# Optimization experiments

Hardware: AMD Instinct MI355X
Metric: run time of the kernel (lower is better)

Reference implementation:

```python
import jax, jax.numpy as jnp
import numpy as np

B, T, SDIM, NIV = 8192, 128, 6, 6
ENC = 16            # features per microstructure encoder
MDIM = 2 * ENC      # 32
HID = 256
DT = 0.01
IN_DIM = SDIM * 2 + NIV + MDIM  # 50


def _lin_init(key, fan_in, fan_out):
    # torch nn.Linear default: U(-1/sqrt(fan_in), 1/sqrt(fan_in)); stored as [in, out]
    k1, k2 = jax.random.split(key)
    bound = 1.0 / np.sqrt(fan_in)
    W = jax.random.uniform(k1, (fan_in, fan_out), jnp.float32, -bound, bound)
    b = jax.random.uniform(k2, (fan_out,), jnp.float32, -bound, bound)
    return W, b


def setup_inputs() -> dict:
    key = jax.random.key(0)
    ks = jax.random.split(key, 10)
    e = jax.random.normal(ks[0], (B, T, SDIM), jnp.float32)
    e_dot = jax.random.normal(ks[1], (B, T, SDIM), jnp.float32)
    E = jax.random.uniform(ks[2], (B, 1), jnp.float32)
    nu = jax.random.uniform(ks[3], (B, 1), jnp.float32)
    We, be = _lin_init(ks[4], 1, ENC)
    Wn, bn = _lin_init(ks[5], 1, ENC)
    Wen1, ben1 = _lin_init(ks[6], IN_DIM, HID)
    Wen2, ben2 = _lin_init(ks[7], HID, 1)
    Wd1, bd1 = _lin_init(ks[8], IN_DIM, HID)
    Wd2, bd2 = _lin_init(ks[9], HID, NIV)
    return {"e": e, "e_dot": e_dot, "E": E, "nu": nu,
            "We": We, "be": be, "Wn": Wn, "bn": bn,
            "Wen1": Wen1, "ben1": ben1, "Wen2": Wen2, "ben2": ben2,
            "Wd1": Wd1, "bd1": bd1, "Wd2": Wd2, "bd2": bd2}


def _mlp(x, W1, b1, W2, b2):
    return jnp.maximum(x @ W1 + b1, 0.0) @ W2 + b2


def reference(e, e_dot, E, nu, We, be, Wn, bn, Wen1, ben1, Wen2, ben2, Wd1, bd1, Wd2, bd2):
    # microstructure features; original recomputes every step but inputs are constant
    mf = jnp.concatenate([E @ We + be, nu @ Wn + bn], axis=-1)  # [B, MDIM]
    e_t = jnp.moveaxis(e, 1, 0)        # [T, B, SDIM]
    ed_t = jnp.moveaxis(e_dot, 1, 0)   # [T, B, SDIM]
    xi0 = jnp.zeros((e.shape[0], NIV), e.dtype)

    def step(xi, inp):
        et, edt = inp
        x = jnp.concatenate([et, edt, xi, mf], axis=-1)       # [B, IN_DIM]
        s = _mlp(x, Wen1, ben1, Wen2, ben2)[..., 0]           # [B] energy -> stress
        kin = _mlp(x, Wd1, bd1, Wd2, bd2)                     # [B, NIV]
        return xi + DT * kin, (s, xi)  # explicit Euler update; emit xi BEFORE update

    _, (stress, xi_all) = jax.lax.scan(step, xi0, (e_t, ed_t))
    # stress: [T, B] -> [B, T]; xi_all: [T, B, NIV] -> [B, T, NIV] (xi[:,0] == 0)
    return jnp.moveaxis(stress, 0, 1), jnp.moveaxis(xi_all, 0, 1)
```

## Files before the change

kernel.cpp:

```cpp
#include <hip/hip_runtime.h>

#define BN   8192
#define TN   128
#define HIDN 256
#define DTC  0.01f

typedef float v2f __attribute__((ext_vector_type(2)));

#define DPP_ADD(v, ctrl, rmask)                                                 \
    v += __int_as_float(__builtin_amdgcn_update_dpp(                            \
            0, __float_as_int(v), ctrl, rmask, 0xf, true))

#define WAVE_SUM(v) do {                                                        \
    DPP_ADD(v, 0x111, 0xf);                                     \
    DPP_ADD(v, 0x112, 0xf);                                     \
    DPP_ADD(v, 0x114, 0xf);                                     \
    DPP_ADD(v, 0x118, 0xf);            \
    DPP_ADD(v, 0x142, 0xa);   \
    DPP_ADD(v, 0x143, 0xc);              \
} while (0)

#define LANE_SUM(v) __int_as_float(__builtin_amdgcn_readlane(__float_as_int(v), 63))

__global__ __launch_bounds__(256, 2)
void visco_kernel(const float* __restrict__ e,    const float* __restrict__ ed,
                  const float* __restrict__ Earr, const float* __restrict__ nuarr,
                  const float* __restrict__ We,   const float* __restrict__ be,
                  const float* __restrict__ Wn,   const float* __restrict__ bn,
                  const float* __restrict__ Wen1, const float* __restrict__ ben1,
                  const float* __restrict__ Wen2, const float* __restrict__ ben2,
                  const float* __restrict__ Wd1,  const float* __restrict__ bd1,
                  const float* __restrict__ Wd2,  const float* __restrict__ bd2,
                  float* __restrict__ out)
{
    const int lane = threadIdx.x & 63;
    const int wv   = threadIdx.x >> 6;
    const int b    = (blockIdx.x << 2) + wv;

    v2f   wP[2][4][9];
    float cst[2][4];
    float w2s[4];
    float w2k[4][6];

    const float Eb  = Earr[b];
    const float nub = nuarr[b];

    #pragma unroll
    for (int u = 0; u < 4; ++u) {
        const int j = (u << 6) + lane;
        #pragma unroll
        for (int kk = 0; kk < 9; ++kk) {
            wP[0][u][kk] = v2f{Wen1[(2 * kk) * HIDN + j], Wen1[(2 * kk + 1) * HIDN + j]};
            wP[1][u][kk] = v2f{Wd1 [(2 * kk) * HIDN + j], Wd1 [(2 * kk + 1) * HIDN + j]};
        }
        float c0 = ben1[j];
        float c1 = bd1[j];
        #pragma unroll
        for (int k = 0; k < 16; ++k) {
            const float m = fmaf(Eb, We[k], be[k]);
            c0 = fmaf(m, Wen1[(18 + k) * HIDN + j], c0);
            c1 = fmaf(m, Wd1 [(18 + k) * HIDN + j], c1);
        }
        #pragma unroll
        for (int k = 0; k < 16; ++k) {
            const float m = fmaf(nub, Wn[k], bn[k]);
            c0 = fmaf(m, Wen1[(34 + k) * HIDN + j], c0);
            c1 = fmaf(m, Wd1 [(34 + k) * HIDN + j], c1);
        }
        cst[0][u] = c0;
        cst[1][u] = c1;
        w2s[u] = Wen2[j];
        #pragma unroll
        for (int i = 0; i < 6; ++i) w2k[u][i] = Wd2[j * 6 + i];
    }

    const float ben2v = ben2[0];
    float bd2v[6];
    #pragma unroll
    for (int i = 0; i < 6; ++i) bd2v[i] = bd2[i];

    v2f xi01 = v2f{0.f, 0.f}, xi23 = v2f{0.f, 0.f}, xi45 = v2f{0.f, 0.f};

    const v2f* ep = (const v2f*)(e  + (size_t)b * (TN * 6));
    const v2f* dp = (const v2f*)(ed + (size_t)b * (TN * 6));
    float* outS = out + (size_t)b * TN;
    float* outX = out + (size_t)BN * TN + (size_t)b * (TN * 6);

    v2f e0 = ep[0], e1 = ep[1], e2 = ep[2];
    v2f d0 = dp[0], d1 = dp[1], d2 = dp[2];

    for (int t = 0; t < TN; ++t) {
        const v2f x0 = e0, x1 = e1, x2v = e2;
        const v2f x3 = d0, x4 = d1, x5 = d2;

        const int tn = (t + 1 < TN) ? t + 1 : t;
        e0 = ep[tn * 3 + 0]; e1 = ep[tn * 3 + 1]; e2 = ep[tn * 3 + 2];
        d0 = dp[tn * 3 + 0]; d1 = dp[tn * 3 + 1]; d2 = dp[tn * 3 + 2];

        float ps  = 0.f;
        float pk0 = 0.f, pk1 = 0.f, pk2 = 0.f, pk3 = 0.f, pk4 = 0.f, pk5 = 0.f;

        #pragma unroll
        for (int u = 0; u < 4; ++u) {
            v2f hp = v2f{cst[0][u], 0.f};
            v2f gp = v2f{cst[1][u], 0.f};
            hp = __builtin_elementwise_fma(x0,   wP[0][u][0], hp);
            gp = __builtin_elementwise_fma(x0,   wP[1][u][0], gp);
            hp = __builtin_elementwise_fma(x1,   wP[0][u][1], hp);
            gp = __builtin_elementwise_fma(x1,   wP[1][u][1], gp);
            hp = __builtin_elementwise_fma(x2v,  wP[0][u][2], hp);
            gp = __builtin_elementwise_fma(x2v,  wP[1][u][2], gp);
            hp = __builtin_elementwise_fma(x3,   wP[0][u][3], hp);
            gp = __builtin_elementwise_fma(x3,   wP[1][u][3], gp);
            hp = __builtin_elementwise_fma(x4,   wP[0][u][4], hp);
            gp = __builtin_elementwise_fma(x4,   wP[1][u][4], gp);
            hp = __builtin_elementwise_fma(x5,   wP[0][u][5], hp);
            gp = __builtin_elementwise_fma(x5,   wP[1][u][5], gp);
            hp = __builtin_elementwise_fma(xi01, wP[0][u][6], hp);
            gp = __builtin_elementwise_fma(xi01, wP[1][u][6], gp);
            hp = __builtin_elementwise_fma(xi23, wP[0][u][7], hp);
            gp = __builtin_elementwise_fma(xi23, wP[1][u][7], gp);
            hp = __builtin_elementwise_fma(xi45, wP[0][u][8], hp);
            gp = __builtin_elementwise_fma(xi45, wP[1][u][8], gp);

            const float h = fmaxf(hp.x + hp.y, 0.f);
            const float g = fmaxf(gp.x + gp.y, 0.f);
            ps  = fmaf(h, w2s[u],    ps);
            pk0 = fmaf(g, w2k[u][0], pk0);
            pk1 = fmaf(g, w2k[u][1], pk1);
            pk2 = fmaf(g, w2k[u][2], pk2);
            pk3 = fmaf(g, w2k[u][3], pk3);
            pk4 = fmaf(g, w2k[u][4], pk4);
            pk5 = fmaf(g, w2k[u][5], pk5);
        }

        WAVE_SUM(ps);
        WAVE_SUM(pk0); WAVE_SUM(pk1); WAVE_SUM(pk2);
        WAVE_SUM(pk3); WAVE_SUM(pk4); WAVE_SUM(pk5);
        const float sS  = LANE_SUM(ps);
        const float s0  = LANE_SUM(pk0);
        const float s1  = LANE_SUM(pk1);
        const float s2  = LANE_SUM(pk2);
        const float s3  = LANE_SUM(pk3);
        const float s4  = LANE_SUM(pk4);
        const float s5  = LANE_SUM(pk5);

        const float xw = (lane == 0) ? xi01.x :
                         (lane == 1) ? xi01.y :
                         (lane == 2) ? xi23.x :
                         (lane == 3) ? xi23.y :
                         (lane == 4) ? xi45.x : xi45.y;
        if (lane < 6)  outX[t * 6 + lane] = xw;
        if (lane == 6) outS[t] = sS + ben2v;

        xi01.x = fmaf(DTC, s0 + bd2v[0], xi01.x);
        xi01.y = fmaf(DTC, s1 + bd2v[1], xi01.y);
        xi23.x = fmaf(DTC, s2 + bd2v[2], xi23.x);
        xi23.y = fmaf(DTC, s3 + bd2v[3], xi23.y);
        xi45.x = fmaf(DTC, s4 + bd2v[4], xi45.x);
        xi45.y = fmaf(DTC, s5 + bd2v[5], xi45.y);
    }
}

extern "C" void kernel_launch(void* const* d_in, const int* in_sizes, int n_in,
                              void* d_out, int out_size, void* d_ws, size_t ws_size,
                              hipStream_t stream) {
    const float* e    = (const float*)d_in[0];
    const float* ed   = (const float*)d_in[1];
    const float* E    = (const float*)d_in[2];
    const float* nu   = (const float*)d_in[3];
    const float* We   = (const float*)d_in[4];
    const float* be   = (const float*)d_in[5];
    const float* Wn   = (const float*)d_in[6];
    const float* bn   = (const float*)d_in[7];
    const float* Wen1 = (const float*)d_in[8];
    const float* ben1 = (const float*)d_in[9];
    const float* Wen2 = (const float*)d_in[10];
    const float* ben2 = (const float*)d_in[11];
    const float* Wd1  = (const float*)d_in[12];
    const float* bd1  = (const float*)d_in[13];
    const float* Wd2  = (const float*)d_in[14];
    const float* bd2  = (const float*)d_in[15];
    float* out = (float*)d_out;

    dim3 grid(BN / 4);
    dim3 block(256);
    visco_kernel<<<grid, block, 0, stream>>>(e, ed, E, nu, We, be, Wn, bn,
                                             Wen1, ben1, Wen2, ben2,
                                             Wd1, bd1, Wd2, bd2, out);
}
```

Baseline: 631.5 us.

## Stage per-step inputs in lanes and broadcast via readlane instead of per-step loads

```diff
diff --git a/kernel.cpp b/kernel.cpp
--- a/kernel.cpp
+++ b/kernel.cpp
@@ -15,14 +15,16 @@
     DPP_ADD(v, 0x111, 0xf);                                     \
     DPP_ADD(v, 0x112, 0xf);                                     \
     DPP_ADD(v, 0x114, 0xf);                                     \
-    DPP_ADD(v, 0x118, 0xf);            \
-    DPP_ADD(v, 0x142, 0xa);   \
-    DPP_ADD(v, 0x143, 0xc);              \
+    DPP_ADD(v, 0x118, 0xf);                                     \
+    DPP_ADD(v, 0x142, 0xa);                                   \
+    DPP_ADD(v, 0x143, 0xc);            \
 } while (0)
 
-#define LANE_SUM(v) __int_as_float(__builtin_amdgcn_readlane(__float_as_int(v), 63))
-
-__global__ __launch_bounds__(256, 2)
+#define LANE_SUM(v)  __int_as_float(__builtin_amdgcn_readlane(__float_as_int(v), 63))
+#define RDLANE(v, l) __int_as_float(__builtin_amdgcn_readlane(__float_as_int(v), (l)))
+#define KEEP(x) asm volatile("" : "+v"(x))
+
+__global__ __launch_bounds__(256, 1)
 void visco_kernel(const float* __restrict__ e,    const float* __restrict__ ed,
                   const float* __restrict__ Earr, const float* __restrict__ nuarr,
                   const float* __restrict__ We,   const float* __restrict__ be,
@@ -38,7 +40,7 @@
     const int b    = (blockIdx.x << 2) + wv;
 
     v2f   wP[2][4][9];
-    float cst[2][4];
+    v2f   cstP[2][4];
     float w2s[4];
     float w2k[4][6];
 
@@ -67,98 +69,115 @@
             c0 = fmaf(m, Wen1[(34 + k) * HIDN + j], c0);
             c1 = fmaf(m, Wd1 [(34 + k) * HIDN + j], c1);
         }
-        cst[0][u] = c0;
-        cst[1][u] = c1;
+        cstP[0][u] = v2f{c0, 0.f};
+        cstP[1][u] = v2f{c1, 0.f};
         w2s[u] = Wen2[j];
         #pragma unroll
         for (int i = 0; i < 6; ++i) w2k[u][i] = Wd2[j * 6 + i];
+    }
+
+    #pragma unroll
+    for (int u = 0; u < 4; ++u) {
+        #pragma unroll
+        for (int kk = 0; kk < 9; ++kk) {
+            KEEP(wP[0][u][kk].x); KEEP(wP[0][u][kk].y);
+            KEEP(wP[1][u][kk].x); KEEP(wP[1][u][kk].y);
+        }
+        #pragma unroll
+        for (int i = 0; i < 6; ++i) KEEP(w2k[u][i]);
+        KEEP(cstP[0][u].x); KEEP(cstP[1][u].x); KEEP(w2s[u]);
     }
 
     const float ben2v = ben2[0];
     float bd2v[6];
     #pragma unroll
-    for (int i = 0; i < 6; ++i) bd2v[i] = bd2[i];
+    for (int i = 0; i < 6; ++i) { bd2v[i] = bd2[i]; KEEP(bd2v[i]); }
 
     v2f xi01 = v2f{0.f, 0.f}, xi23 = v2f{0.f, 0.f}, xi45 = v2f{0.f, 0.f};
 
-    const v2f* ep = (const v2f*)(e  + (size_t)b * (TN * 6));
-    const v2f* dp = (const v2f*)(ed + (size_t)b * (TN * 6));
+    const float* eb = e  + (size_t)b * (TN * 6);
+    const float* db = ed + (size_t)b * (TN * 6);
     float* outS = out + (size_t)b * TN;
     float* outX = out + (size_t)BN * TN + (size_t)b * (TN * 6);
 
-    v2f e0 = ep[0], e1 = ep[1], e2 = ep[2];
-    v2f d0 = dp[0], d1 = dp[1], d2 = dp[2];
-
-    for (int t = 0; t < TN; ++t) {
-        const v2f x0 = e0, x1 = e1, x2v = e2;
-        const v2f x3 = d0, x4 = d1, x5 = d2;
-
-        const int tn = (t + 1 < TN) ? t + 1 : t;
-        e0 = ep[tn * 3 + 0]; e1 = ep[tn * 3 + 1]; e2 = ep[tn * 3 + 2];
-        d0 = dp[tn * 3 + 0]; d1 = dp[tn * 3 + 1]; d2 = dp[tn * 3 + 2];
-
-        float ps  = 0.f;
-        float pk0 = 0.f, pk1 = 0.f, pk2 = 0.f, pk3 = 0.f, pk4 = 0.f, pk5 = 0.f;
-
-        #pragma unroll
-        for (int u = 0; u < 4; ++u) {
-            v2f hp = v2f{cst[0][u], 0.f};
-            v2f gp = v2f{cst[1][u], 0.f};
-            hp = __builtin_elementwise_fma(x0,   wP[0][u][0], hp);
-            gp = __builtin_elementwise_fma(x0,   wP[1][u][0], gp);
-            hp = __builtin_elementwise_fma(x1,   wP[0][u][1], hp);
-            gp = __builtin_elementwise_fma(x1,   wP[1][u][1], gp);
-            hp = __builtin_elementwise_fma(x2v,  wP[0][u][2], hp);
-            gp = __builtin_elementwise_fma(x2v,  wP[1][u][2], gp);
-            hp = __builtin_elementwise_fma(x3,   wP[0][u][3], hp);
-            gp = __builtin_elementwise_fma(x3,   wP[1][u][3], gp);
-            hp = __builtin_elementwise_fma(x4,   wP[0][u][4], hp);
-            gp = __builtin_elementwise_fma(x4,   wP[1][u][4], gp);
-            hp = __builtin_elementwise_fma(x5,   wP[0][u][5], hp);
-            gp = __builtin_elementwise_fma(x5,   wP[1][u][5], gp);
-            hp = __builtin_elementwise_fma(xi01, wP[0][u][6], hp);
-            gp = __builtin_elementwise_fma(xi01, wP[1][u][6], gp);
-            hp = __builtin_elementwise_fma(xi23, wP[0][u][7], hp);
-            gp = __builtin_elementwise_fma(xi23, wP[1][u][7], gp);
-            hp = __builtin_elementwise_fma(xi45, wP[0][u][8], hp);
-            gp = __builtin_elementwise_fma(xi45, wP[1][u][8], gp);
-
-            const float h = fmaxf(hp.x + hp.y, 0.f);
-            const float g = fmaxf(gp.x + gp.y, 0.f);
-            ps  = fmaf(h, w2s[u],    ps);
-            pk0 = fmaf(g, w2k[u][0], pk0);
-            pk1 = fmaf(g, w2k[u][1], pk1);
-            pk2 = fmaf(g, w2k[u][2], pk2);
-            pk3 = fmaf(g, w2k[u][3], pk3);
-            pk4 = fmaf(g, w2k[u][4], pk4);
-            pk5 = fmaf(g, w2k[u][5], pk5);
-        }
-
-        WAVE_SUM(ps);
-        WAVE_SUM(pk0); WAVE_SUM(pk1); WAVE_SUM(pk2);
-        WAVE_SUM(pk3); WAVE_SUM(pk4); WAVE_SUM(pk5);
-        const float sS  = LANE_SUM(ps);
-        const float s0  = LANE_SUM(pk0);
-        const float s1  = LANE_SUM(pk1);
-        const float s2  = LANE_SUM(pk2);
-        const float s3  = LANE_SUM(pk3);
-        const float s4  = LANE_SUM(pk4);
-        const float s5  = LANE_SUM(pk5);
-
-        const float xw = (lane == 0) ? xi01.x :
-                         (lane == 1) ? xi01.y :
-                         (lane == 2) ? xi23.x :
-                         (lane == 3) ? xi23.y :
-                         (lane == 4) ? xi45.x : xi45.y;
-        if (lane < 6)  outX[t * 6 + lane] = xw;
-        if (lane == 6) outS[t] = sS + ben2v;
-
-        xi01.x = fmaf(DTC, s0 + bd2v[0], xi01.x);
-        xi01.y = fmaf(DTC, s1 + bd2v[1], xi01.y);
-        xi23.x = fmaf(DTC, s2 + bd2v[2], xi23.x);
-        xi23.y = fmaf(DTC, s3 + bd2v[3], xi23.y);
-        xi45.x = fmaf(DTC, s4 + bd2v[4], xi45.x);
-        xi45.y = fmaf(DTC, s5 + bd2v[5], xi45.y);
+    for (int half = 0; half < 2; ++half) {
+        float sE[6], sD[6];
+        const int base = ((half << 6) + lane) * 6;
+        #pragma unroll
+        for (int r = 0; r < 6; ++r) { sE[r] = eb[base + r]; sD[r] = db[base + r]; }
+
+        #pragma unroll 2
+        for (int t2 = 0; t2 < 64; ++t2) {
+            const int t = (half << 6) + t2;
+
+            const v2f x0 = v2f{RDLANE(sE[0], t2), RDLANE(sE[1], t2)};
+            const v2f x1 = v2f{RDLANE(sE[2], t2), RDLANE(sE[3], t2)};
+            const v2f x2 = v2f{RDLANE(sE[4], t2), RDLANE(sE[5], t2)};
+            const v2f x3 = v2f{RDLANE(sD[0], t2), RDLANE(sD[1], t2)};
+            const v2f x4 = v2f{RDLANE(sD[2], t2), RDLANE(sD[3], t2)};
+            const v2f x5 = v2f{RDLANE(sD[4], t2), RDLANE(sD[5], t2)};
+
+            float ps  = 0.f;
+            float pk0 = 0.f, pk1 = 0.f, pk2 = 0.f, pk3 = 0.f, pk4 = 0.f, pk5 = 0.f;
+
+            #pragma unroll
+            for (int u = 0; u < 4; ++u) {
+                v2f hp = __builtin_elementwise_fma(x0, wP[0][u][0], cstP[0][u]);
+                v2f gp = __builtin_elementwise_fma(x0, wP[1][u][0], cstP[1][u]);
+                hp = __builtin_elementwise_fma(x1,   wP[0][u][1], hp);
+                gp = __builtin_elementwise_fma(x1,   wP[1][u][1], gp);
+                hp = __builtin_elementwise_fma(x2,   wP[0][u][2], hp);
+                gp = __builtin_elementwise_fma(x2,   wP[1][u][2], gp);
+                hp = __builtin_elementwise_fma(x3,   wP[0][u][3], hp);
+                gp = __builtin_elementwise_fma(x3,   wP[1][u][3], gp);
+                hp = __builtin_elementwise_fma(x4,   wP[0][u][4], hp);
+                gp = __builtin_elementwise_fma(x4,   wP[1][u][4], gp);
+                hp = __builtin_elementwise_fma(x5,   wP[0][u][5], hp);
+                gp = __builtin_elementwise_fma(x5,   wP[1][u][5], gp);
+                hp = __builtin_elementwise_fma(xi01, wP[0][u][6], hp);
+                gp = __builtin_elementwise_fma(xi01, wP[1][u][6], gp);
+                hp = __builtin_elementwise_fma(xi23, wP[0][u][7], hp);
+                gp = __builtin_elementwise_fma(xi23, wP[1][u][7], gp);
+                hp = __builtin_elementwise_fma(xi45, wP[0][u][8], hp);
+                gp = __builtin_elementwise_fma(xi45, wP[1][u][8], gp);
+
+                const float h = fmaxf(hp.x + hp.y, 0.f);
+                const float g = fmaxf(gp.x + gp.y, 0.f);
+                ps  = fmaf(h, w2s[u],    ps);
+                pk0 = fmaf(g, w2k[u][0], pk0);
+                pk1 = fmaf(g, w2k[u][1], pk1);
+                pk2 = fmaf(g, w2k[u][2], pk2);
+                pk3 = fmaf(g, w2k[u][3], pk3);
+                pk4 = fmaf(g, w2k[u][4], pk4);
+                pk5 = fmaf(g, w2k[u][5], pk5);
+            }
+
+            WAVE_SUM(ps);
+            WAVE_SUM(pk0); WAVE_SUM(pk1); WAVE_SUM(pk2);
+            WAVE_SUM(pk3); WAVE_SUM(pk4); WAVE_SUM(pk5);
+            const float sS = LANE_SUM(ps);
+            const float s0 = LANE_SUM(pk0);
+            const float s1 = LANE_SUM(pk1);
+            const float s2 = LANE_SUM(pk2);
+            const float s3 = LANE_SUM(pk3);
+            const float s4 = LANE_SUM(pk4);
+            const float s5 = LANE_SUM(pk5);
+
+            const float xw = (lane == 0) ? xi01.x :
+                             (lane == 1) ? xi01.y :
+                             (lane == 2) ? xi23.x :
+                             (lane == 3) ? xi23.y :
+                             (lane == 4) ? xi45.x : xi45.y;
+            if (lane < 6)  outX[t * 6 + lane] = xw;
+            if (lane == 6) outS[t] = sS + ben2v;
+
+            xi01.x = fmaf(DTC, s0 + bd2v[0], xi01.x);
+            xi01.y = fmaf(DTC, s1 + bd2v[1], xi01.y);
+            xi23.x = fmaf(DTC, s2 + bd2v[2], xi23.x);
+            xi23.y = fmaf(DTC, s3 + bd2v[3], xi23.y);
+            xi45.x = fmaf(DTC, s4 + bd2v[4], xi45.x);
+            xi45.y = fmaf(DTC, s5 + bd2v[5], xi45.y);
+        }
     }
 }
 
```

Measured after the change: 572.6 us. -9.3%, faster.
